# Optimization experiments

Hardware: AMD Instinct MI355X
Metric: run time of the kernel (lower is better)

## Reference

```python
import jax, jax.numpy as jnp
import numpy as np

OUT_FEATURES = 14336
IN_FEATURES = 4096
BLOCK = 64

NF4_MAPPING = jnp.array([
    -1.0, -0.6961928009986877, -0.5250730514526367, -0.39491748809814453,
    -0.28444138169288635, -0.18477343022823334, -0.09105003625154495, 0.0,
    0.07958029955625534, 0.16093020141124725, 0.24611230194568634,
    0.33791524171829224, 0.44070982933044434, 0.5626170039176941,
    0.7229568362236023, 1.0], dtype=jnp.float32)


def setup_inputs() -> dict:
    key = jax.random.key(0)
    k1, k2, k3, k4, k5 = jax.random.split(key, 5)
    x = jax.random.normal(k1, (8192, IN_FEATURES), dtype=jnp.float32)
    w_packed = jax.random.randint(k2, (OUT_FEATURES * IN_FEATURES // 2,), 0, 256, dtype=jnp.int32)
    w_absmax = jax.random.uniform(k3, (OUT_FEATURES * IN_FEATURES // BLOCK,), dtype=jnp.float32)
    b_packed = jax.random.randint(k4, (OUT_FEATURES // 2,), 0, 256, dtype=jnp.int32)
    b_absmax = jax.random.uniform(k5, (OUT_FEATURES // BLOCK,), dtype=jnp.float32)
    return {"x": x, "w_packed": w_packed, "w_absmax": w_absmax,
            "b_packed": b_packed, "b_absmax": b_absmax}


def _nf4_dequantize(packed, absmax, shape):
    # Each byte holds two 4-bit codes: (hi*16 + lo); unpack in (hi, lo) order
    # exactly like torch.stack([w // 16, w % 16], dim=1).view(-1).
    codes = jnp.stack([packed // 16, packed % 16], axis=-1).reshape(-1)
    vals = NF4_MAPPING[codes]                       # [N] dequantized in [-1, 1]
    blocks = vals.reshape(-1, BLOCK) * absmax.reshape(-1, 1)  # per-block rescale
    return blocks.reshape(shape)


def reference(x, w_packed, w_absmax, b_packed, b_absmax):
    weight = _nf4_dequantize(w_packed, w_absmax, (OUT_FEATURES, IN_FEATURES))
    bias = _nf4_dequantize(b_packed, b_absmax, (OUT_FEATURES,))
    return jnp.matmul(x, weight.T) + bias
```

## Files before the change

### kernel.cpp

```cpp
#include <hip/hip_runtime.h>

typedef unsigned short u16;
typedef signed char s8;
typedef __attribute__((ext_vector_type(4))) float f32x4;
typedef __attribute__((ext_vector_type(4))) int i32x4;

#define M_ROWS 8192
#define N_OUT  14336
#define K_IN   4096
#define NTILE  64

__constant__ float NF4_TAB[16] = {
    -1.0f, -0.6961928009986877f, -0.5250730514526367f, -0.39491748809814453f,
    -0.28444138169288635f, -0.18477343022823334f, -0.09105003625154495f, 0.0f,
    0.07958029955625534f, 0.16093020141124725f, 0.24611230194568634f,
    0.33791524171829224f, 0.44070982933044434f, 0.5626170039176941f,
    0.7229568362236023f, 1.0f};

static __device__ __forceinline__ void async_load16(const void* g, void* l) {
  __builtin_amdgcn_global_load_lds(
      (const __attribute__((address_space(1))) void*)g,
      (__attribute__((address_space(3))) void*)l, 16, 0, 0);
}

__global__ __launch_bounds__(256) void quant_w_kernel(
    const int* __restrict__ wp, const float* __restrict__ wa,
    s8* __restrict__ wout, float* __restrict__ sn) {
  const int n = blockIdx.x;
  const int t = threadIdx.x, lane = t & 63, wid = t >> 6;
  const i32x4 p0 = __builtin_nontemporal_load(
      reinterpret_cast<const i32x4*>(wp) + (size_t)n * 512 + 2 * t);
  const i32x4 p1 = __builtin_nontemporal_load(
      reinterpret_cast<const i32x4*>(wp) + (size_t)n * 512 + 2 * t + 1);
  const float am = wa[n * 64 + (t >> 2)];

  float v[16];
  int pv[8] = {p0.x, p0.y, p0.z, p0.w, p1.x, p1.y, p1.z, p1.w};
  float mx = 0.0f;
#pragma unroll
  for (int i = 0; i < 8; ++i) {
    v[2 * i]     = NF4_TAB[(pv[i] >> 4) & 15];
    v[2 * i + 1] = NF4_TAB[pv[i] & 15];
  }
#pragma unroll
  for (int i = 0; i < 16; ++i) mx = fmaxf(mx, fabsf(v[i]));
  mx *= am;
#pragma unroll
  for (int off = 32; off; off >>= 1) mx = fmaxf(mx, __shfl_xor(mx, off));
  __shared__ float red[4];
  if (lane == 0) red[wid] = mx;
  __syncthreads();
  const float colmax = fmaxf(fmaxf(red[0], red[1]), fmaxf(red[2], red[3]));
  const float inv = colmax > 0.0f ? (127.0f * am) / colmax : 0.0f;

  union { s8 c[16]; i32x4 q; } o;
#pragma unroll
  for (int i = 0; i < 16; ++i) o.c[i] = (s8)(int)rintf(v[i] * inv);
  reinterpret_cast<i32x4*>(wout)[(size_t)n * 256 + t] = o.q;
  if (t == 0) sn[n] = colmax * (1.0f / 127.0f);
}

__global__ __launch_bounds__(256) void quant_x_kernel(
    const float* __restrict__ x, s8* __restrict__ xi8,
    float* __restrict__ sxr) {
  const int row = blockIdx.x;
  const int tid = threadIdx.x, lane = tid & 63, wid = tid >> 6;
  const float4* xr = reinterpret_cast<const float4*>(x + (size_t)row * 4096);
  float4 v[4];
  float mx = 0.0f;
#pragma unroll
  for (int i = 0; i < 4; ++i) {
    v[i] = xr[tid * 4 + i];
    mx = fmaxf(mx, fmaxf(fmaxf(fabsf(v[i].x), fabsf(v[i].y)),
                         fmaxf(fabsf(v[i].z), fabsf(v[i].w))));
  }
#pragma unroll
  for (int off = 32; off; off >>= 1) mx = fmaxf(mx, __shfl_xor(mx, off));
  __shared__ float red[4];
  if (lane == 0) red[wid] = mx;
  __syncthreads();
  mx = fmaxf(fmaxf(red[0], red[1]), fmaxf(red[2], red[3]));
  float rs = mx > 0.0f ? 127.0f / mx : 0.0f;
  union { s8 c[16]; i32x4 q; } o;
#pragma unroll
  for (int i = 0; i < 4; ++i) {
    o.c[4 * i + 0] = (s8)(int)rintf(v[i].x * rs);
    o.c[4 * i + 1] = (s8)(int)rintf(v[i].y * rs);
    o.c[4 * i + 2] = (s8)(int)rintf(v[i].z * rs);
    o.c[4 * i + 3] = (s8)(int)rintf(v[i].w * rs);
  }
  reinterpret_cast<i32x4*>(xi8 + (size_t)row * 4096)[tid] = o.q;
  if (tid == 0) sxr[row] = mx * (1.0f / 127.0f);
}

__global__ __launch_bounds__(512, 4) void gemm_nf4_i8(
    const s8* __restrict__ A,
    const s8* __restrict__ B,
    float* __restrict__ C, const int* __restrict__ bp,
    const float* __restrict__ ba, const float* __restrict__ sn,
    const float* __restrict__ sxr) {
  constexpr int K = K_IN, N = N_OUT;
  extern __shared__ char smem[];
  char* sA = smem;
  char* sB = smem + 32768;

  const int tid = threadIdx.x;
  const int w = tid >> 6, lane = tid & 63;
  const int r = lane & 15, kq = lane >> 4;
  const int wr = w >> 1, wc = w & 1;

  int bid = blockIdx.x;
  int cpx = gridDim.x >> 3;
  int wg = (bid & 7) * cpx + (bid >> 3);
  int grp = wg / 896;
  int rem = wg - grp * 896;
  int nt = rem >> 3;
  int mt = grp * 8 + (rem & 7);
  const size_t m0 = (size_t)mt * 256, n0 = (size_t)nt * 128;

  const s8* gA = A + m0 * K;
  const s8* gB = B + n0 * K;

  const int cswz = ((kq ^ ((r >> 1) & 3)) << 4);
  const int cg16 = (((lane & 3) ^ ((lane >> 3) & 3)) << 4);
  const int rl = lane >> 2;

  const s8* stA0 = gA + (size_t)(w * 16 + rl) * K + cg16;
  const s8* stA1 = gA + (size_t)(128 + w * 16 + rl) * K + cg16;
  const s8* stB0 = gB + (size_t)(w * 16 + rl) * K + cg16;

  i32x4 acc[4][4] = {};
  i32x4 aF[4];

#define BAR() __builtin_amdgcn_s_barrier()
#define VM(n) asm volatile("s_waitcnt vmcnt(" #n ")" ::: "memory")

#define STAGE_AB(P, s) do {                                                   \
    async_load16(stA0 + (size_t)(s) * 64, sA + (P) * 16384 + w * 1024);       \
    async_load16(stA1 + (size_t)(s) * 64, sA + (P) * 16384 + 8192 + w * 1024);\
    async_load16(stB0 + (size_t)(s) * 64, sB + (P) * 8192 + w * 1024);        \
  } while (0)

#define READ_A(P) do {                                                       \
    const char* pa_ = sA + (P) * 16384 + (wr * 64 + r) * 64;                 \
    _Pragma("unroll")                                                        \
    for (int m_ = 0; m_ < 4; ++m_)                                           \
      aF[m_] = *(const i32x4*)(pa_ + m_ * 1024 + cswz);                      \
  } while (0)

#define MFMA_ALL(P) do {                                                     \
    const char* pb_ = sB + (P) * 8192 + (wc * 64 + r) * 64;                  \
    __builtin_amdgcn_s_setprio(1);                                           \
    _Pragma("unroll")                                                        \
    for (int n_ = 0; n_ < 4; ++n_) {                                         \
      i32x4 bF_ = *(const i32x4*)(pb_ + n_ * 1024 + cswz);                   \
      _Pragma("unroll")                                                      \
      for (int m_ = 0; m_ < 4; ++m_)                                         \
        acc[m_][n_] = __builtin_amdgcn_mfma_i32_16x16x64_i8(                 \
            aF[m_], bF_, acc[m_][n_], 0, 0, 0);                              \
    }                                                                        \
    __builtin_amdgcn_s_setprio(0);                                           \
  } while (0)

#define BODY(s, P, DO_STAGE, DO_VMBAR) do {                                  \
    READ_A(P);                                                               \
    if (DO_STAGE) STAGE_AB((P) ^ 1, (s) + 1);                                \
    MFMA_ALL(P);                                                             \
    if (DO_VMBAR) { VM(0); BAR(); }                                          \
  } while (0)

  STAGE_AB(0, 0);
  VM(0); BAR();

  for (int s = 0; s < NTILE - 2; s += 2) {
    BODY(s, 0, 1, 1);
    BODY(s + 1, 1, 1, 1);
  }
  BODY(NTILE - 2, 0, 1, 1);
  BODY(NTILE - 1, 1, 0, 0);

  float bias[4], snv[4];
#pragma unroll
  for (int ni = 0; ni < 4; ++ni) {
    int col = (int)n0 + wc * 64 + ni * 16 + r;
    int byte = bp[col >> 1];
    int code = (col & 1) ? (byte & 15) : ((byte >> 4) & 15);
    bias[ni] = NF4_TAB[code] * ba[col >> 6];
    snv[ni] = sn[col];
  }
#pragma unroll
  for (int mi = 0; mi < 4; ++mi) {
    size_t row0 = m0 + wr * 64 + mi * 16 + kq * 4;
    const f32x4 sxv = *reinterpret_cast<const f32x4*>(sxr + row0);
#pragma unroll
    for (int ni = 0; ni < 4; ++ni) {
      size_t col = n0 + wc * 64 + ni * 16 + r;
#pragma unroll
      for (int j = 0; j < 4; ++j)
        C[(row0 + j) * N + col] =
            (float)acc[mi][ni][j] * (snv[ni] * sxv[j]) + bias[ni];
    }
  }
#undef BODY
#undef MFMA_ALL
#undef READ_A
#undef STAGE_AB
#undef VM
#undef BAR
}

extern "C" void kernel_launch(void* const* d_in, const int* in_sizes, int n_in,
                              void* d_out, int out_size, void* d_ws,
                              size_t ws_size, hipStream_t stream) {
  const float* x  = (const float*)d_in[0];
  const int* wp   = (const int*)d_in[1];
  const float* wa = (const float*)d_in[2];
  const int* bp   = (const int*)d_in[3];
  const float* ba = (const float*)d_in[4];
  float* out = (float*)d_out;

  s8* Wi8 = (s8*)d_ws;
  s8* Xi8 = Wi8 + (size_t)N_OUT * K_IN;
  float* sn  = (float*)(Xi8 + (size_t)M_ROWS * K_IN);
  float* sxr = sn + N_OUT;

  quant_w_kernel<<<N_OUT, 256, 0, stream>>>(wp, wa, Wi8, sn);
  quant_x_kernel<<<M_ROWS, 256, 0, stream>>>(x, Xi8, sxr);

  hipFuncSetAttribute(reinterpret_cast<const void*>(gemm_nf4_i8),
                      hipFuncAttributeMaxDynamicSharedMemorySize, 49152);
  gemm_nf4_i8<<<3584, 512, 49152, stream>>>(Xi8, Wi8, out, bp, ba, sn, sxr);
}
```

Measured before the change: 615.5 us.

## Switch GEMM to 32x32x32 int8 MFMA and merge quantization kernels

Replaces the 16x16x64 int8 MFMA tiling with 32x32x32 int8 MFMAs. Each wave now holds a 2x2 grid of 32x32 accumulators and issues fewer, larger matrix ops per K tile, with the LDS fragment reads and epilogue mapping rewritten to match the new output layout. It also fuses the weight and activation quantization kernels into a single launch to save one launch and overlap the two passes. It drops the s_setprio hints, and correctness depends on the new swizzle and lane mapping matching the 32x32 operand layout.

Measured after the change: 653.1 us. 1.06x slower.

```diff
diff --git a/kernel.cpp b/kernel.cpp
--- a/kernel.cpp
+++ b/kernel.cpp
@@ -4,6 +4,7 @@
 typedef signed char s8;
 typedef __attribute__((ext_vector_type(4))) float f32x4;
 typedef __attribute__((ext_vector_type(4))) int i32x4;
+typedef __attribute__((ext_vector_type(16))) int i32x16;
 
 #define M_ROWS 8192
 #define N_OUT  14336
@@ -23,74 +24,73 @@
       (__attribute__((address_space(3))) void*)l, 16, 0, 0);
 }
 
-__global__ __launch_bounds__(256) void quant_w_kernel(
+__global__ __launch_bounds__(256) void quant_wx_kernel(
     const int* __restrict__ wp, const float* __restrict__ wa,
-    s8* __restrict__ wout, float* __restrict__ sn) {
-  const int n = blockIdx.x;
-  const int t = threadIdx.x, lane = t & 63, wid = t >> 6;
-  const i32x4 p0 = __builtin_nontemporal_load(
-      reinterpret_cast<const i32x4*>(wp) + (size_t)n * 512 + 2 * t);
-  const i32x4 p1 = __builtin_nontemporal_load(
-      reinterpret_cast<const i32x4*>(wp) + (size_t)n * 512 + 2 * t + 1);
-  const float am = wa[n * 64 + (t >> 2)];
-
-  float v[16];
-  int pv[8] = {p0.x, p0.y, p0.z, p0.w, p1.x, p1.y, p1.z, p1.w};
-  float mx = 0.0f;
-#pragma unroll
-  for (int i = 0; i < 8; ++i) {
-    v[2 * i]     = NF4_TAB[(pv[i] >> 4) & 15];
-    v[2 * i + 1] = NF4_TAB[pv[i] & 15];
-  }
-#pragma unroll
-  for (int i = 0; i < 16; ++i) mx = fmaxf(mx, fabsf(v[i]));
-  mx *= am;
-#pragma unroll
-  for (int off = 32; off; off >>= 1) mx = fmaxf(mx, __shfl_xor(mx, off));
-  __shared__ float red[4];
-  if (lane == 0) red[wid] = mx;
-  __syncthreads();
-  const float colmax = fmaxf(fmaxf(red[0], red[1]), fmaxf(red[2], red[3]));
-  const float inv = colmax > 0.0f ? (127.0f * am) / colmax : 0.0f;
-
-  union { s8 c[16]; i32x4 q; } o;
-#pragma unroll
-  for (int i = 0; i < 16; ++i) o.c[i] = (s8)(int)rintf(v[i] * inv);
-  reinterpret_cast<i32x4*>(wout)[(size_t)n * 256 + t] = o.q;
-  if (t == 0) sn[n] = colmax * (1.0f / 127.0f);
-}
-
-__global__ __launch_bounds__(256) void quant_x_kernel(
+    s8* __restrict__ wout, float* __restrict__ sn,
     const float* __restrict__ x, s8* __restrict__ xi8,
     float* __restrict__ sxr) {
-  const int row = blockIdx.x;
-  const int tid = threadIdx.x, lane = tid & 63, wid = tid >> 6;
-  const float4* xr = reinterpret_cast<const float4*>(x + (size_t)row * 4096);
-  float4 v[4];
-  float mx = 0.0f;
-#pragma unroll
-  for (int i = 0; i < 4; ++i) {
-    v[i] = xr[tid * 4 + i];
-    mx = fmaxf(mx, fmaxf(fmaxf(fabsf(v[i].x), fabsf(v[i].y)),
-                         fmaxf(fabsf(v[i].z), fabsf(v[i].w))));
-  }
-#pragma unroll
-  for (int off = 32; off; off >>= 1) mx = fmaxf(mx, __shfl_xor(mx, off));
   __shared__ float red[4];
-  if (lane == 0) red[wid] = mx;
-  __syncthreads();
-  mx = fmaxf(fmaxf(red[0], red[1]), fmaxf(red[2], red[3]));
-  float rs = mx > 0.0f ? 127.0f / mx : 0.0f;
-  union { s8 c[16]; i32x4 q; } o;
-#pragma unroll
-  for (int i = 0; i < 4; ++i) {
-    o.c[4 * i + 0] = (s8)(int)rintf(v[i].x * rs);
-    o.c[4 * i + 1] = (s8)(int)rintf(v[i].y * rs);
-    o.c[4 * i + 2] = (s8)(int)rintf(v[i].z * rs);
-    o.c[4 * i + 3] = (s8)(int)rintf(v[i].w * rs);
-  }
-  reinterpret_cast<i32x4*>(xi8 + (size_t)row * 4096)[tid] = o.q;
-  if (tid == 0) sxr[row] = mx * (1.0f / 127.0f);
+  const int t = threadIdx.x, lane = t & 63, wid = t >> 6;
+
+  if (blockIdx.x < N_OUT) {
+    const int n = blockIdx.x;
+    const i32x4 p0 = __builtin_nontemporal_load(
+        reinterpret_cast<const i32x4*>(wp) + (size_t)n * 512 + 2 * t);
+    const i32x4 p1 = __builtin_nontemporal_load(
+        reinterpret_cast<const i32x4*>(wp) + (size_t)n * 512 + 2 * t + 1);
+    const float am = wa[n * 64 + (t >> 2)];
+
+    float v[16];
+    int pv[8] = {p0.x, p0.y, p0.z, p0.w, p1.x, p1.y, p1.z, p1.w};
+    float mx = 0.0f;
+#pragma unroll
+    for (int i = 0; i < 8; ++i) {
+      v[2 * i]     = NF4_TAB[(pv[i] >> 4) & 15];
+      v[2 * i + 1] = NF4_TAB[pv[i] & 15];
+    }
+#pragma unroll
+    for (int i = 0; i < 16; ++i) mx = fmaxf(mx, fabsf(v[i]));
+    mx *= am;
+#pragma unroll
+    for (int off = 32; off; off >>= 1) mx = fmaxf(mx, __shfl_xor(mx, off));
+    if (lane == 0) red[wid] = mx;
+    __syncthreads();
+    const float colmax = fmaxf(fmaxf(red[0], red[1]), fmaxf(red[2], red[3]));
+    const float inv = colmax > 0.0f ? (127.0f * am) / colmax : 0.0f;
+
+    union { s8 c[16]; i32x4 q; } o;
+#pragma unroll
+    for (int i = 0; i < 16; ++i) o.c[i] = (s8)(int)rintf(v[i] * inv);
+    reinterpret_cast<i32x4*>(wout)[(size_t)n * 256 + t] = o.q;
+    if (t == 0) sn[n] = colmax * (1.0f / 127.0f);
+  } else {
+    const int row = blockIdx.x - N_OUT;
+    const float4* xr = reinterpret_cast<const float4*>(x + (size_t)row * 4096);
+    float4 v[4];
+    float mx = 0.0f;
+#pragma unroll
+    for (int i = 0; i < 4; ++i) {
+      v[i] = xr[t * 4 + i];
+      mx = fmaxf(mx, fmaxf(fmaxf(fabsf(v[i].x), fabsf(v[i].y)),
+                           fmaxf(fabsf(v[i].z), fabsf(v[i].w))));
+    }
+#pragma unroll
+    for (int off = 32; off; off >>= 1) mx = fmaxf(mx, __shfl_xor(mx, off));
+    if (lane == 0) red[wid] = mx;
+    __syncthreads();
+    mx = fmaxf(fmaxf(red[0], red[1]), fmaxf(red[2], red[3]));
+    float rs = mx > 0.0f ? 127.0f / mx : 0.0f;
+    union { s8 c[16]; i32x4 q; } o;
+#pragma unroll
+    for (int i = 0; i < 4; ++i) {
+      o.c[4 * i + 0] = (s8)(int)rintf(v[i].x * rs);
+      o.c[4 * i + 1] = (s8)(int)rintf(v[i].y * rs);
+      o.c[4 * i + 2] = (s8)(int)rintf(v[i].z * rs);
+      o.c[4 * i + 3] = (s8)(int)rintf(v[i].w * rs);
+    }
+    reinterpret_cast<i32x4*>(xi8 + (size_t)row * 4096)[t] = o.q;
+    if (t == 0) sxr[row] = mx * (1.0f / 127.0f);
+  }
 }
 
 __global__ __launch_bounds__(512, 4) void gemm_nf4_i8(
@@ -106,7 +106,7 @@
 
   const int tid = threadIdx.x;
   const int w = tid >> 6, lane = tid & 63;
-  const int r = lane & 15, kq = lane >> 4;
+  const int r32 = lane & 31, hi = lane >> 5;
   const int wr = w >> 1, wc = w & 1;
 
   int bid = blockIdx.x;
@@ -121,7 +121,9 @@
   const s8* gA = A + m0 * K;
   const s8* gB = B + n0 * K;
 
-  const int cswz = ((kq ^ ((r >> 1) & 3)) << 4);
+  const int gm = (r32 >> 1) & 3;
+  const int cswz0 = ((0 + hi) ^ gm) << 4;
+  const int cswz1 = ((2 + hi) ^ gm) << 4;
   const int cg16 = (((lane & 3) ^ ((lane >> 3) & 3)) << 4);
   const int rl = lane >> 2;
 
@@ -129,8 +131,8 @@
   const s8* stA1 = gA + (size_t)(128 + w * 16 + rl) * K + cg16;
   const s8* stB0 = gB + (size_t)(w * 16 + rl) * K + cg16;
 
-  i32x4 acc[4][4] = {};
-  i32x4 aF[4];
+  i32x16 acc[2][2] = {};
+  i32x4 aF[2][2];
 
 #define BAR() __builtin_amdgcn_s_barrier()
 #define VM(n) asm volatile("s_waitcnt vmcnt(" #n ")" ::: "memory")
@@ -142,24 +144,28 @@
   } while (0)
 
 #define READ_A(P) do {                                                       \
-    const char* pa_ = sA + (P) * 16384 + (wr * 64 + r) * 64;                 \
+    const char* pa_ = sA + (P) * 16384 + (wr * 64 + r32) * 64;               \
+    aF[0][0] = *(const i32x4*)(pa_ + cswz0);                                 \
+    aF[0][1] = *(const i32x4*)(pa_ + cswz1);                                 \
+    aF[1][0] = *(const i32x4*)(pa_ + 2048 + cswz0);                          \
+    aF[1][1] = *(const i32x4*)(pa_ + 2048 + cswz1);                          \
+  } while (0)
+
+#define MFMA_ALL(P) do {                                                     \
+    const char* pb_ = sB + (P) * 8192 + (wc * 64 + r32) * 64;                \
     _Pragma("unroll")                                                        \
-    for (int m_ = 0; m_ < 4; ++m_)                                           \
-      aF[m_] = *(const i32x4*)(pa_ + m_ * 1024 + cswz);                      \
-  } while (0)
-
-#define MFMA_ALL(P) do {                                                     \
-    const char* pb_ = sB + (P) * 8192 + (wc * 64 + r) * 64;                  \
-    __builtin_amdgcn_s_setprio(1);                                           \
-    _Pragma("unroll")                                                        \
-    for (int n_ = 0; n_ < 4; ++n_) {                                         \
-      i32x4 bF_ = *(const i32x4*)(pb_ + n_ * 1024 + cswz);                   \
-      _Pragma("unroll")                                                      \
-      for (int m_ = 0; m_ < 4; ++m_)                                         \
-        acc[m_][n_] = __builtin_amdgcn_mfma_i32_16x16x64_i8(                 \
-            aF[m_], bF_, acc[m_][n_], 0, 0, 0);                              \
+    for (int n_ = 0; n_ < 2; ++n_) {                                         \
+      i32x4 b0_ = *(const i32x4*)(pb_ + n_ * 2048 + cswz0);                  \
+      acc[0][n_] = __builtin_amdgcn_mfma_i32_32x32x32_i8(                    \
+          aF[0][0], b0_, acc[0][n_], 0, 0, 0);                               \
+      acc[1][n_] = __builtin_amdgcn_mfma_i32_32x32x32_i8(                    \
+          aF[1][0], b0_, acc[1][n_], 0, 0, 0);                               \
+      i32x4 b1_ = *(const i32x4*)(pb_ + n_ * 2048 + cswz1);                  \
+      acc[0][n_] = __builtin_amdgcn_mfma_i32_32x32x32_i8(                    \
+          aF[0][1], b1_, acc[0][n_], 0, 0, 0);                               \
+      acc[1][n_] = __builtin_amdgcn_mfma_i32_32x32x32_i8(                    \
+          aF[1][1], b1_, acc[1][n_], 0, 0, 0);                               \
     }                                                                        \
-    __builtin_amdgcn_s_setprio(0);                                           \
   } while (0)
 
 #define BODY(s, P, DO_STAGE, DO_VMBAR) do {                                  \
@@ -179,26 +185,29 @@
   BODY(NTILE - 2, 0, 1, 1);
   BODY(NTILE - 1, 1, 0, 0);
 
-  float bias[4], snv[4];
-#pragma unroll
-  for (int ni = 0; ni < 4; ++ni) {
-    int col = (int)n0 + wc * 64 + ni * 16 + r;
+  float bias[2], snv[2];
+#pragma unroll
+  for (int ni = 0; ni < 2; ++ni) {
+    int col = (int)n0 + wc * 64 + ni * 32 + r32;
     int byte = bp[col >> 1];
     int code = (col & 1) ? (byte & 15) : ((byte >> 4) & 15);
     bias[ni] = NF4_TAB[code] * ba[col >> 6];
     snv[ni] = sn[col];
   }
 #pragma unroll
-  for (int mi = 0; mi < 4; ++mi) {
-    size_t row0 = m0 + wr * 64 + mi * 16 + kq * 4;
-    const f32x4 sxv = *reinterpret_cast<const f32x4*>(sxr + row0);
-#pragma unroll
-    for (int ni = 0; ni < 4; ++ni) {
-      size_t col = n0 + wc * 64 + ni * 16 + r;
-#pragma unroll
-      for (int j = 0; j < 4; ++j)
-        C[(row0 + j) * N + col] =
-            (float)acc[mi][ni][j] * (snv[ni] * sxv[j]) + bias[ni];
+  for (int mi = 0; mi < 2; ++mi) {
+#pragma unroll
+    for (int g = 0; g < 4; ++g) {
+      size_t row0 = m0 + wr * 64 + mi * 32 + g * 8 + 4 * hi;
+      const f32x4 sxv = *reinterpret_cast<const f32x4*>(sxr + row0);
+#pragma unroll
+      for (int ni = 0; ni < 2; ++ni) {
+        size_t col = n0 + wc * 64 + ni * 32 + r32;
+#pragma unroll
+        for (int j = 0; j < 4; ++j)
+          C[(row0 + j) * N + col] =
+              (float)acc[mi][ni][g * 4 + j] * (snv[ni] * sxv[j]) + bias[ni];
+      }
     }
   }
 #undef BODY
@@ -224,8 +233,8 @@
   float* sn  = (float*)(Xi8 + (size_t)M_ROWS * K_IN);
   float* sxr = sn + N_OUT;
 
-  quant_w_kernel<<<N_OUT, 256, 0, stream>>>(wp, wa, Wi8, sn);
-  quant_x_kernel<<<M_ROWS, 256, 0, stream>>>(x, Xi8, sxr);
+  quant_wx_kernel<<<N_OUT + M_ROWS, 256, 0, stream>>>(
+      wp, wa, Wi8, sn, x, Xi8, sxr);
 
   hipFuncSetAttribute(reinterpret_cast<const void*>(gemm_nf4_i8),
                       hipFuncAttributeMaxDynamicSharedMemorySize, 49152);
```

## Load B fragments directly to registers and merge quantization kernels

Applied to the files above, without the earlier changes.

The GEMM stops staging the B (weight) tile through LDS. Each wave now loads its B fragments straight from global memory into a double-buffered register array, and A is still staged via async LDS loads. This cuts LDS from 48KB to 32KB and removes the B LDS reads, but it adds uncoalesced per-lane global loads, duplicates B reads across waves that share wc, and raises register pressure. It also drops the setprio hints. Separately, the W and X quantization kernels are fused into one launch to save a kernel launch and let the two overlap.

After: 1.158 ms. +88.1%, slower.

```diff
diff --git a/kernel.cpp b/kernel.cpp
--- a/kernel.cpp
+++ b/kernel.cpp
@@ -23,74 +23,73 @@
       (__attribute__((address_space(3))) void*)l, 16, 0, 0);
 }
 
-__global__ __launch_bounds__(256) void quant_w_kernel(
+__global__ __launch_bounds__(256) void quant_wx_kernel(
     const int* __restrict__ wp, const float* __restrict__ wa,
-    s8* __restrict__ wout, float* __restrict__ sn) {
-  const int n = blockIdx.x;
-  const int t = threadIdx.x, lane = t & 63, wid = t >> 6;
-  const i32x4 p0 = __builtin_nontemporal_load(
-      reinterpret_cast<const i32x4*>(wp) + (size_t)n * 512 + 2 * t);
-  const i32x4 p1 = __builtin_nontemporal_load(
-      reinterpret_cast<const i32x4*>(wp) + (size_t)n * 512 + 2 * t + 1);
-  const float am = wa[n * 64 + (t >> 2)];
-
-  float v[16];
-  int pv[8] = {p0.x, p0.y, p0.z, p0.w, p1.x, p1.y, p1.z, p1.w};
-  float mx = 0.0f;
-#pragma unroll
-  for (int i = 0; i < 8; ++i) {
-    v[2 * i]     = NF4_TAB[(pv[i] >> 4) & 15];
-    v[2 * i + 1] = NF4_TAB[pv[i] & 15];
-  }
-#pragma unroll
-  for (int i = 0; i < 16; ++i) mx = fmaxf(mx, fabsf(v[i]));
-  mx *= am;
-#pragma unroll
-  for (int off = 32; off; off >>= 1) mx = fmaxf(mx, __shfl_xor(mx, off));
-  __shared__ float red[4];
-  if (lane == 0) red[wid] = mx;
-  __syncthreads();
-  const float colmax = fmaxf(fmaxf(red[0], red[1]), fmaxf(red[2], red[3]));
-  const float inv = colmax > 0.0f ? (127.0f * am) / colmax : 0.0f;
-
-  union { s8 c[16]; i32x4 q; } o;
-#pragma unroll
-  for (int i = 0; i < 16; ++i) o.c[i] = (s8)(int)rintf(v[i] * inv);
-  reinterpret_cast<i32x4*>(wout)[(size_t)n * 256 + t] = o.q;
-  if (t == 0) sn[n] = colmax * (1.0f / 127.0f);
-}
-
-__global__ __launch_bounds__(256) void quant_x_kernel(
+    s8* __restrict__ wout, float* __restrict__ sn,
     const float* __restrict__ x, s8* __restrict__ xi8,
     float* __restrict__ sxr) {
-  const int row = blockIdx.x;
-  const int tid = threadIdx.x, lane = tid & 63, wid = tid >> 6;
-  const float4* xr = reinterpret_cast<const float4*>(x + (size_t)row * 4096);
-  float4 v[4];
-  float mx = 0.0f;
-#pragma unroll
-  for (int i = 0; i < 4; ++i) {
-    v[i] = xr[tid * 4 + i];
-    mx = fmaxf(mx, fmaxf(fmaxf(fabsf(v[i].x), fabsf(v[i].y)),
-                         fmaxf(fabsf(v[i].z), fabsf(v[i].w))));
-  }
-#pragma unroll
-  for (int off = 32; off; off >>= 1) mx = fmaxf(mx, __shfl_xor(mx, off));
   __shared__ float red[4];
-  if (lane == 0) red[wid] = mx;
-  __syncthreads();
-  mx = fmaxf(fmaxf(red[0], red[1]), fmaxf(red[2], red[3]));
-  float rs = mx > 0.0f ? 127.0f / mx : 0.0f;
-  union { s8 c[16]; i32x4 q; } o;
-#pragma unroll
-  for (int i = 0; i < 4; ++i) {
-    o.c[4 * i + 0] = (s8)(int)rintf(v[i].x * rs);
-    o.c[4 * i + 1] = (s8)(int)rintf(v[i].y * rs);
-    o.c[4 * i + 2] = (s8)(int)rintf(v[i].z * rs);
-    o.c[4 * i + 3] = (s8)(int)rintf(v[i].w * rs);
-  }
-  reinterpret_cast<i32x4*>(xi8 + (size_t)row * 4096)[tid] = o.q;
-  if (tid == 0) sxr[row] = mx * (1.0f / 127.0f);
+  const int t = threadIdx.x, lane = t & 63, wid = t >> 6;
+
+  if (blockIdx.x < N_OUT) {
+    const int n = blockIdx.x;
+    const i32x4 p0 = __builtin_nontemporal_load(
+        reinterpret_cast<const i32x4*>(wp) + (size_t)n * 512 + 2 * t);
+    const i32x4 p1 = __builtin_nontemporal_load(
+        reinterpret_cast<const i32x4*>(wp) + (size_t)n * 512 + 2 * t + 1);
+    const float am = wa[n * 64 + (t >> 2)];
+
+    float v[16];
+    int pv[8] = {p0.x, p0.y, p0.z, p0.w, p1.x, p1.y, p1.z, p1.w};
+    float mx = 0.0f;
+#pragma unroll
+    for (int i = 0; i < 8; ++i) {
+      v[2 * i]     = NF4_TAB[(pv[i] >> 4) & 15];
+      v[2 * i + 1] = NF4_TAB[pv[i] & 15];
+    }
+#pragma unroll
+    for (int i = 0; i < 16; ++i) mx = fmaxf(mx, fabsf(v[i]));
+    mx *= am;
+#pragma unroll
+    for (int off = 32; off; off >>= 1) mx = fmaxf(mx, __shfl_xor(mx, off));
+    if (lane == 0) red[wid] = mx;
+    __syncthreads();
+    const float colmax = fmaxf(fmaxf(red[0], red[1]), fmaxf(red[2], red[3]));
+    const float inv = colmax > 0.0f ? (127.0f * am) / colmax : 0.0f;
+
+    union { s8 c[16]; i32x4 q; } o;
+#pragma unroll
+    for (int i = 0; i < 16; ++i) o.c[i] = (s8)(int)rintf(v[i] * inv);
+    reinterpret_cast<i32x4*>(wout)[(size_t)n * 256 + t] = o.q;
+    if (t == 0) sn[n] = colmax * (1.0f / 127.0f);
+  } else {
+    const int row = blockIdx.x - N_OUT;
+    const float4* xr = reinterpret_cast<const float4*>(x + (size_t)row * 4096);
+    float4 v[4];
+    float mx = 0.0f;
+#pragma unroll
+    for (int i = 0; i < 4; ++i) {
+      v[i] = xr[t * 4 + i];
+      mx = fmaxf(mx, fmaxf(fmaxf(fabsf(v[i].x), fabsf(v[i].y)),
+                           fmaxf(fabsf(v[i].z), fabsf(v[i].w))));
+    }
+#pragma unroll
+    for (int off = 32; off; off >>= 1) mx = fmaxf(mx, __shfl_xor(mx, off));
+    if (lane == 0) red[wid] = mx;
+    __syncthreads();
+    mx = fmaxf(fmaxf(red[0], red[1]), fmaxf(red[2], red[3]));
+    float rs = mx > 0.0f ? 127.0f / mx : 0.0f;
+    union { s8 c[16]; i32x4 q; } o;
+#pragma unroll
+    for (int i = 0; i < 4; ++i) {
+      o.c[4 * i + 0] = (s8)(int)rintf(v[i].x * rs);
+      o.c[4 * i + 1] = (s8)(int)rintf(v[i].y * rs);
+      o.c[4 * i + 2] = (s8)(int)rintf(v[i].z * rs);
+      o.c[4 * i + 3] = (s8)(int)rintf(v[i].w * rs);
+    }
+    reinterpret_cast<i32x4*>(xi8 + (size_t)row * 4096)[t] = o.q;
+    if (t == 0) sxr[row] = mx * (1.0f / 127.0f);
+  }
 }
 
 __global__ __launch_bounds__(512, 4) void gemm_nf4_i8(
@@ -102,7 +101,6 @@
   constexpr int K = K_IN, N = N_OUT;
   extern __shared__ char smem[];
   char* sA = smem;
-  char* sB = smem + 32768;
 
   const int tid = threadIdx.x;
   const int w = tid >> 6, lane = tid & 63;
@@ -127,49 +125,49 @@
 
   const s8* stA0 = gA + (size_t)(w * 16 + rl) * K + cg16;
   const s8* stA1 = gA + (size_t)(128 + w * 16 + rl) * K + cg16;
-  const s8* stB0 = gB + (size_t)(w * 16 + rl) * K + cg16;
+  const s8* gBf[4];
+#pragma unroll
+  for (int n_ = 0; n_ < 4; ++n_)
+    gBf[n_] = gB + (size_t)(wc * 64 + n_ * 16 + r) * K + kq * 16;
 
   i32x4 acc[4][4] = {};
-  i32x4 aF[4];
+  i32x4 bFr[2][4];
 
 #define BAR() __builtin_amdgcn_s_barrier()
 #define VM(n) asm volatile("s_waitcnt vmcnt(" #n ")" ::: "memory")
 
-#define STAGE_AB(P, s) do {                                                   \
+#define STAGE_A(P, s) do {                                                    \
     async_load16(stA0 + (size_t)(s) * 64, sA + (P) * 16384 + w * 1024);       \
     async_load16(stA1 + (size_t)(s) * 64, sA + (P) * 16384 + 8192 + w * 1024);\
-    async_load16(stB0 + (size_t)(s) * 64, sB + (P) * 8192 + w * 1024);        \
-  } while (0)
-
-#define READ_A(P) do {                                                       \
+  } while (0)
+
+#define PREFETCH_B(PB, s) do {                                               \
+    _Pragma("unroll")                                                        \
+    for (int n_ = 0; n_ < 4; ++n_)                                           \
+      bFr[PB][n_] = *reinterpret_cast<const i32x4*>(                         \
+          gBf[n_] + (size_t)(s) * 64);                                       \
+  } while (0)
+
+#define MFMA_ALL(P) do {                                                     \
     const char* pa_ = sA + (P) * 16384 + (wr * 64 + r) * 64;                 \
     _Pragma("unroll")                                                        \
-    for (int m_ = 0; m_ < 4; ++m_)                                           \
-      aF[m_] = *(const i32x4*)(pa_ + m_ * 1024 + cswz);                      \
-  } while (0)
-
-#define MFMA_ALL(P) do {                                                     \
-    const char* pb_ = sB + (P) * 8192 + (wc * 64 + r) * 64;                  \
-    __builtin_amdgcn_s_setprio(1);                                           \
-    _Pragma("unroll")                                                        \
-    for (int n_ = 0; n_ < 4; ++n_) {                                         \
-      i32x4 bF_ = *(const i32x4*)(pb_ + n_ * 1024 + cswz);                   \
+    for (int m_ = 0; m_ < 4; ++m_) {                                         \
+      i32x4 aF_ = *(const i32x4*)(pa_ + m_ * 1024 + cswz);                   \
       _Pragma("unroll")                                                      \
-      for (int m_ = 0; m_ < 4; ++m_)                                         \
+      for (int n_ = 0; n_ < 4; ++n_)                                         \
         acc[m_][n_] = __builtin_amdgcn_mfma_i32_16x16x64_i8(                 \
-            aF[m_], bF_, acc[m_][n_], 0, 0, 0);                              \
+            aF_, bFr[P][n_], acc[m_][n_], 0, 0, 0);                          \
     }                                                                        \
-    __builtin_amdgcn_s_setprio(0);                                           \
-  } while (0)
-
-#define BODY(s, P, DO_STAGE, DO_VMBAR) do {                                  \
-    READ_A(P);                                                               \
-    if (DO_STAGE) STAGE_AB((P) ^ 1, (s) + 1);                                \
+  } while (0)
+
+#define BODY(s, P, DO_NEXT, DO_VMBAR) do {                                   \
+    if (DO_NEXT) { PREFETCH_B((P) ^ 1, (s) + 1); STAGE_A((P) ^ 1, (s) + 1); }\
     MFMA_ALL(P);                                                             \
     if (DO_VMBAR) { VM(0); BAR(); }                                          \
   } while (0)
 
-  STAGE_AB(0, 0);
+  STAGE_A(0, 0);
+  PREFETCH_B(0, 0);
   VM(0); BAR();
 
   for (int s = 0; s < NTILE - 2; s += 2) {
@@ -203,8 +201,8 @@
   }
 #undef BODY
 #undef MFMA_ALL
-#undef READ_A
-#undef STAGE_AB
+#undef PREFETCH_B
+#undef STAGE_A
 #undef VM
 #undef BAR
 }
@@ -224,10 +222,10 @@
   float* sn  = (float*)(Xi8 + (size_t)M_ROWS * K_IN);
   float* sxr = sn + N_OUT;
 
-  quant_w_kernel<<<N_OUT, 256, 0, stream>>>(wp, wa, Wi8, sn);
-  quant_x_kernel<<<M_ROWS, 256, 0, stream>>>(x, Xi8, sxr);
+  quant_wx_kernel<<<N_OUT + M_ROWS, 256, 0, stream>>>(
+      wp, wa, Wi8, sn, x, Xi8, sxr);
 
   hipFuncSetAttribute(reinterpret_cast<const void*>(gemm_nf4_i8),
-                      hipFuncAttributeMaxDynamicSharedMemorySize, 49152);
-  gemm_nf4_i8<<<3584, 512, 49152, stream>>>(Xi8, Wi8, out, bp, ba, sn, sxr);
-}
+                      hipFuncAttributeMaxDynamicSharedMemorySize, 32768);
+  gemm_nf4_i8<<<3584, 512, 32768, stream>>>(Xi8, Wi8, out, bp, ba, sn, sxr);
+}
```
